# Optimization experiments

Measured on AMD Instinct MI355X. Metric: run time of the kernel, lower is better.

Reference implementation:

```python
import jax, jax.numpy as jnp
import numpy as np


def setup_inputs() -> dict:
    key = jax.random.key(0)
    k1, k2, k3, k4 = jax.random.split(key, 4)
    B, T, E, D = 4, 4096, 2048, 128
    x = jax.random.normal(k1, (B, T, E), dtype=jnp.float32)
    # nn.Linear(E, D, bias=False): y = x @ W where W is [E, D]
    scale = 1.0 / np.sqrt(E)
    Wq = jax.random.normal(k2, (E, D), dtype=jnp.float32) * scale
    Wk = jax.random.normal(k3, (E, D), dtype=jnp.float32) * scale
    Wv = jax.random.normal(k4, (E, D), dtype=jnp.float32) * scale
    return {"x": x, "Wq": Wq, "Wk": Wk, "Wv": Wv}


def reference(x, Wq, Wk, Wv):
    # Single attention head, prefill path (kv_cache=None, T_q == T_k).
    D = Wq.shape[1]
    Q = jnp.einsum('bte,ed->btd', x, Wq)
    K = jnp.einsum('bte,ed->btd', x, Wk)
    V = jnp.einsum('bte,ed->btd', x, Wv)
    scores = jnp.einsum('bqd,bkd->bqk', Q, K) / jnp.sqrt(jnp.float32(D))
    T = x.shape[1]
    causal = jnp.tril(jnp.ones((T, T), dtype=bool))  # [T_q, T_k]
    scores = jnp.where(causal[None, :, :], scores, -jnp.inf)
    attn = jax.nn.softmax(scores, axis=-1)
    out = jnp.einsum('bqk,bkd->bqd', attn, V)
    return out
```

## Files before the change

### kernel.cpp

```cpp
#include <hip/hip_runtime.h>
#include <hip/hip_bf16.h>

typedef short bf16x8 __attribute__((ext_vector_type(8)));
typedef float f32x4  __attribute__((ext_vector_type(4)));

#define T_SEQ 4096
#define NB    4
#define E_DIM 2048
#define D_DIM 128
#define M_TOT (NB * T_SEQ)
#define NCHUNK 4
#define CHUNK_KT 16
#define SM_SHIFT 12.0f

__device__ __forceinline__ ushort f2bf(float f) {
  union { float f; unsigned u; } c; c.f = f;
  unsigned u = c.u;
  unsigned r = (u + 0x7FFFu + ((u >> 16) & 1u)) >> 16;
  return (ushort)r;
}
__device__ __forceinline__ float bf2f(ushort u) {
  union { unsigned u; float f; } c; c.u = ((unsigned)u) << 16;
  return c.f;
}
__device__ __forceinline__ bf16x8 cvt8(const float4& lo, const float4& hi) {
  union { __hip_bfloat162 h; ushort u[2]; } t;
  union { ushort u[8]; bf16x8 v; } r;
  t.h = __float22bfloat162_rn(make_float2(lo.x, lo.y)); r.u[0] = t.u[0]; r.u[1] = t.u[1];
  t.h = __float22bfloat162_rn(make_float2(lo.z, lo.w)); r.u[2] = t.u[0]; r.u[3] = t.u[1];
  t.h = __float22bfloat162_rn(make_float2(hi.x, hi.y)); r.u[4] = t.u[0]; r.u[5] = t.u[1];
  t.h = __float22bfloat162_rn(make_float2(hi.z, hi.w)); r.u[6] = t.u[0]; r.u[7] = t.u[1];
  return r.v;
}

__device__ __forceinline__ void gl2lds16(const void* g, void* l) {
  __builtin_amdgcn_global_load_lds(
      (const __attribute__((address_space(1))) unsigned int*)g,
      (__attribute__((address_space(3))) unsigned int*)l, 16, 0, 0);
}

__global__ __launch_bounds__(256) void build_wt(const float* __restrict__ Wq,
                                                const float* __restrict__ Wk,
                                                const float* __restrict__ Wv,
                                                ushort* __restrict__ Wt) {
  __shared__ ushort tile[64][72];
  const int tid = threadIdx.x;
  const int k0 = blockIdx.x * 64, n0 = blockIdx.y * 64, o = blockIdx.z;
  const float* W = (o == 0) ? Wq : ((o == 1) ? Wk : Wv);
  for (int i = 0; i < 4; i++) {
    int c = tid + i * 256;
    int r = c >> 4, c4 = (c & 15) * 4;
    float4 v = *(const float4*)(W + (size_t)(k0 + r) * D_DIM + n0 + c4);
    ushort4 b4;
    b4.x = f2bf(v.x); b4.y = f2bf(v.y); b4.z = f2bf(v.z); b4.w = f2bf(v.w);
    *(ushort4*)(&tile[r][c4]) = b4;
  }
  __syncthreads();
  for (int i = 0; i < 2; i++) {
    int c = tid + i * 256;
    int nn = c >> 3, k8 = (c & 7) * 8;
    ushort tmp[8];
    for (int j = 0; j < 8; j++) tmp[j] = tile[k8 + j][nn];
    *(uint4*)(Wt + (size_t)((o << 7) + n0 + nn) * E_DIM + k0 + k8) = *(const uint4*)tmp;
  }
}

__global__ __launch_bounds__(256) void qkv_gemm(const float* __restrict__ x,
                                                const ushort* __restrict__ Wt,
                                                ushort* __restrict__ Q,
                                                ushort* __restrict__ K,
                                                ushort* __restrict__ V) {
  __shared__ ushort Bs[2][192 * 64];

  const int tid  = threadIdx.x;
  const int wave = tid >> 6, lane = tid & 63;
  const int quad = lane >> 4, l16 = lane & 15;
  const int wm = wave >> 1, wn = wave & 1;
  const int m0 = blockIdx.x * 64;
  const int n0 = blockIdx.y * 192;

  f32x4 acc[2][6] = {};

  const int s_   = wave * 64 + lane;
  const int n_   = s_ >> 3, p_ = s_ & 7;

#define DMA_B(k0_, buf_)                                                        \
  for (int i_ = 0; i_ < 6; i_++) {                                              \
    int slotbase = i_ * 256 + wave * 64;                                        \
    int n = (i_ * 256 >> 3) + n_;       \
    int cg = p_ ^ (n & 7);                                                      \
    gl2lds16(Wt + (size_t)(n0 + n) * E_DIM + (k0_) + cg * 8,                    \
             (char*)(buf_) + (size_t)slotbase * 16);                            \
  }

  DMA_B(0, Bs[0]);
  __syncthreads();

  const float* xbase = x + (size_t)(m0 + wm * 32 + l16) * E_DIM + quad * 8;

  for (int it = 0; it < 32; it++) {
    const int k0 = it * 64;
    if (it < 31) { DMA_B(k0 + 64, Bs[(it + 1) & 1]); }
    const ushort* bs = Bs[it & 1];

    float4 a4[2][2][2];
    for (int mi = 0; mi < 2; mi++)
      for (int kk = 0; kk < 2; kk++) {
        const float* ap = xbase + (size_t)mi * 16 * E_DIM + k0 + kk * 32;
        a4[mi][kk][0] = *(const float4*)ap;
        a4[mi][kk][1] = *(const float4*)(ap + 4);
      }

    for (int kk = 0; kk < 2; kk++) {
      bf16x8 af[2];
      af[0] = cvt8(a4[0][kk][0], a4[0][kk][1]);
      af[1] = cvt8(a4[1][kk][0], a4[1][kk][1]);
      const int sw = ((kk * 4 + quad) ^ (l16 & 7)) * 8;
      for (int ni = 0; ni < 6; ni++) {
        int n = wn * 96 + ni * 16 + l16;
        bf16x8 bf = *(const bf16x8*)(bs + n * 64 + sw);
        acc[0][ni] = __builtin_amdgcn_mfma_f32_16x16x32_bf16(af[0], bf, acc[0][ni], 0, 0, 0);
        acc[1][ni] = __builtin_amdgcn_mfma_f32_16x16x32_bf16(af[1], bf, acc[1][ni], 0, 0, 0);
      }
    }
    __syncthreads();
  }

  for (int mi = 0; mi < 2; mi++)
    for (int ni = 0; ni < 6; ni++) {
      int colall = n0 + wn * 96 + ni * 16 + l16;
      int o = colall >> 7, d = colall & 127;
      ushort* dst = (o == 0) ? Q : ((o == 1) ? K : V);
      for (int r = 0; r < 4; r++) {
        int row = m0 + wm * 32 + mi * 16 + quad * 4 + r;
        dst[(size_t)row * D_DIM + d] = f2bf(acc[mi][ni][r]);
      }
    }
#undef DMA_B
}

__global__ __launch_bounds__(256) void v_transpose(const ushort* __restrict__ V,
                                                   ushort* __restrict__ Vt) {
  __shared__ ushort tile[64][72];
  const int tid = threadIdx.x;
  const int t0 = blockIdx.x * 64, d0 = blockIdx.y * 64, b = blockIdx.z;
  for (int i = 0; i < 2; i++) {
    int c = tid + i * 256;
    int r = c >> 3, cc = (c & 7) * 8;
    *(uint4*)(&tile[r][cc]) = *(const uint4*)(V + (size_t)(b * T_SEQ + t0 + r) * D_DIM + d0 + cc);
  }
  __syncthreads();
  for (int i = 0; i < 2; i++) {
    int c = tid + i * 256;
    int dr = c >> 3, tc = (c & 7) * 8;
    ushort tmp[8];
    for (int j = 0; j < 8; j++) tmp[j] = tile[tc + j][dr];
    *(uint4*)(Vt + (size_t)(b * D_DIM + d0 + dr) * T_SEQ + t0 + tc) = *(const uint4*)tmp;
  }
}

__global__ __launch_bounds__(256) void attn_partial(const ushort* __restrict__ Q,
                                                    const ushort* __restrict__ K,
                                                    const ushort* __restrict__ Vt,
                                                    ushort* __restrict__ Po,
                                                    float* __restrict__ Ll) {
  const int qt = blockIdx.x, cq = blockIdx.y, b = blockIdx.z;
  const int kt0 = cq * CHUNK_KT;
  if (kt0 > qt) return;

  __shared__ ushort Kt[64][136];
  __shared__ ushort Vts[128][72];
  __shared__ ushort Pls[4][16][72];

  const int tid = threadIdx.x;
  const int wave = tid >> 6, lane = tid & 63;
  const int quad = lane >> 4, l16 = lane & 15;

  const int qrow = qt * 64 + wave * 16 + l16;
  bf16x8 qf[4];
  for (int kk = 0; kk < 4; kk++)
    qf[kk] = *(const bf16x8*)(Q + (size_t)(b * T_SEQ + qrow) * D_DIM + kk * 32 + quad * 8);

  bf16x8 ones;
  for (int j = 0; j < 8; j++) ones[j] = (short)0x3F80;

  f32x4 o_acc[8] = {};
  f32x4 lacc = {};
  const float scale2 = 0.08838834764831845f * 1.4426950408889634f;

  const int kt1 = min(qt, kt0 + CHUNK_KT - 1);

  for (int kt = kt0; kt <= kt1; kt++) {
    __syncthreads();
    for (int i = 0; i < 4; i++) {
      int c = tid + i * 256;
      int r = c >> 4, col = (c & 15) * 8;
      *(uint4*)(&Kt[r][col]) = *(const uint4*)(K + (size_t)(b * T_SEQ + kt * 64 + r) * D_DIM + col);
    }
    for (int i = 0; i < 4; i++) {
      int c = tid + i * 256;
      int dr = c >> 3, col = (c & 7) * 8;
      *(uint4*)(&Vts[dr][col]) = *(const uint4*)(Vt + (size_t)(b * D_DIM + dr) * T_SEQ + kt * 64 + col);
    }
    __syncthreads();

    f32x4 s[4] = {};
    for (int kk = 0; kk < 4; kk++) {
      const int kc = kk * 32 + quad * 8;
      for (int ni = 0; ni < 4; ni++) {
        bf16x8 bf = *(const bf16x8*)(&Kt[ni * 16 + l16][kc]);
        s[ni] = __builtin_amdgcn_mfma_f32_16x16x32_bf16(qf[kk], bf, s[ni], 0, 0, 0);
      }
    }
    if (kt == qt) {
      for (int ni = 0; ni < 4; ni++) {
        int kidx = kt * 64 + ni * 16 + l16;
        for (int r = 0; r < 4; r++) {
          int qidx = qt * 64 + wave * 16 + quad * 4 + r;
          float v = (kidx > qidx) ? -1e30f : (s[ni][r] * scale2 - SM_SHIFT);
          s[ni][r] = exp2f(v);
        }
      }
    } else {
      for (int ni = 0; ni < 4; ni++)
        for (int r = 0; r < 4; r++)
          s[ni][r] = exp2f(s[ni][r] * scale2 - SM_SHIFT);
    }
    for (int ni = 0; ni < 4; ni++)
      for (int r = 0; r < 4; r++)
        Pls[wave][quad * 4 + r][ni * 16 + l16] = f2bf(s[ni][r]);
    for (int kk2 = 0; kk2 < 2; kk2++) {
      const int kc = kk2 * 32 + quad * 8;
      bf16x8 pf = *(const bf16x8*)(&Pls[wave][l16][kc]);
      for (int ni = 0; ni < 8; ni++) {
        bf16x8 vf = *(const bf16x8*)(&Vts[ni * 16 + l16][kc]);
        o_acc[ni] = __builtin_amdgcn_mfma_f32_16x16x32_bf16(pf, vf, o_acc[ni], 0, 0, 0);
      }
      lacc = __builtin_amdgcn_mfma_f32_16x16x32_bf16(pf, ones, lacc, 0, 0, 0);
    }
  }

  const int slot = (b * 64 + qt) * NCHUNK + cq;
  for (int ni = 0; ni < 8; ni++)
    for (int r = 0; r < 4; r++) {
      int ql = wave * 16 + quad * 4 + r;
      Po[(size_t)slot * 8192 + ql * D_DIM + ni * 16 + l16] = f2bf(o_acc[ni][r]);
    }
  if (l16 == 0) {
    for (int r = 0; r < 4; r++) {
      int ql = wave * 16 + quad * 4 + r;
      Ll[slot * 64 + ql] = lacc[r];
    }
  }
}

__global__ __launch_bounds__(256) void attn_reduce(const ushort* __restrict__ Po,
                                                   const float* __restrict__ Ll,
                                                   float* __restrict__ out) {
  const int qt = blockIdx.x, b = blockIdx.y;
  const int nc = qt / CHUNK_KT + 1;
  const int tid = threadIdx.x;
  const int row = tid >> 2;
  const int c0  = (tid & 3) * 32;
  const int base_slot = (b * 64 + qt) * NCHUNK;

  float L = 0.f;
  for (int c = 0; c < nc; c++) L += Ll[(base_slot + c) * 64 + row];
  const float inv = 1.0f / L;

  const size_t orow = (size_t)(b * T_SEQ + qt * 64 + row) * D_DIM;
  for (int cc = 0; cc < 32; cc += 8) {
    float a[8] = {0,0,0,0,0,0,0,0};
    for (int c = 0; c < nc; c++) {
      const ushort* p = Po + (size_t)(base_slot + c) * 8192 + row * D_DIM + c0 + cc;
      ushort u[8];
      *(uint4*)u = *(const uint4*)p;
      for (int j = 0; j < 8; j++) a[j] += bf2f(u[j]);
    }
    float4 o0, o1;
    o0.x = a[0] * inv; o0.y = a[1] * inv; o0.z = a[2] * inv; o0.w = a[3] * inv;
    o1.x = a[4] * inv; o1.y = a[5] * inv; o1.z = a[6] * inv; o1.w = a[7] * inv;
    *(float4*)(out + orow + c0 + cc)     = o0;
    *(float4*)(out + orow + c0 + cc + 4) = o1;
  }
}

extern "C" void kernel_launch(void* const* d_in, const int* in_sizes, int n_in,
                              void* d_out, int out_size, void* d_ws, size_t ws_size,
                              hipStream_t stream) {
  const float* x  = (const float*)d_in[0];
  const float* Wq = (const float*)d_in[1];
  const float* Wk = (const float*)d_in[2];
  const float* Wv = (const float*)d_in[3];
  float* out = (float*)d_out;

  ushort* Q  = (ushort*)d_ws;
  ushort* Kb = Q  + (size_t)M_TOT * D_DIM;
  ushort* Vb = Kb + (size_t)M_TOT * D_DIM;
  ushort* Vt = Vb + (size_t)M_TOT * D_DIM;
  ushort* Wt = Vt + (size_t)M_TOT * D_DIM;
  ushort* Po = Wt + (size_t)384 * E_DIM;
  float*  Ll = (float*)(Po + (size_t)NB * 64 * NCHUNK * 8192);

  hipLaunchKernelGGL(build_wt,     dim3(32, 2, 3),       dim3(256), 0, stream, Wq, Wk, Wv, Wt);
  hipLaunchKernelGGL(qkv_gemm,     dim3(256, 2),         dim3(256), 0, stream, x, Wt, Q, Kb, Vb);
  hipLaunchKernelGGL(v_transpose,  dim3(64, 2, 4),       dim3(256), 0, stream, Vb, Vt);
  hipLaunchKernelGGL(attn_partial, dim3(64, NCHUNK, 4),  dim3(256), 0, stream, Q, Kb, Vt, Po, Ll);
  hipLaunchKernelGGL(attn_reduce,  dim3(64, 4),          dim3(256), 0, stream, Po, Ll, out);
}
```

Measured before the change: 299.5 us.

## Pre-pack weights, K and V into MFMA fragment layout and drop LDS staging

```diff
diff --git a/kernel.cpp b/kernel.cpp
--- a/kernel.cpp
+++ b/kernel.cpp
@@ -9,8 +9,6 @@
 #define E_DIM 2048
 #define D_DIM 128
 #define M_TOT (NB * T_SEQ)
-#define NCHUNK 4
-#define CHUNK_KT 16
 #define SM_SHIFT 12.0f
 
 __device__ __forceinline__ ushort f2bf(float f) {
@@ -32,46 +30,47 @@
   t.h = __float22bfloat162_rn(make_float2(hi.z, hi.w)); r.u[6] = t.u[0]; r.u[7] = t.u[1];
   return r.v;
 }
-
-__device__ __forceinline__ void gl2lds16(const void* g, void* l) {
-  __builtin_amdgcn_global_load_lds(
-      (const __attribute__((address_space(1))) unsigned int*)g,
-      (__attribute__((address_space(3))) unsigned int*)l, 16, 0, 0);
-}
-
-__global__ __launch_bounds__(256) void build_wt(const float* __restrict__ Wq,
-                                                const float* __restrict__ Wk,
-                                                const float* __restrict__ Wv,
-                                                ushort* __restrict__ Wt) {
+__device__ __forceinline__ bf16x8 ld_frag(const ushort* p) {
+  union { uint4 q; bf16x8 v; } u;
+  u.q = *(const uint4*)p;
+  return u.v;
+}
+
+__global__ __launch_bounds__(256) void build_wtp(const float* __restrict__ Wq,
+                                                 const float* __restrict__ Wk,
+                                                 const float* __restrict__ Wv,
+                                                 ushort* __restrict__ Wtp) {
   __shared__ ushort tile[64][72];
   const int tid = threadIdx.x;
-  const int k0 = blockIdx.x * 64, n0 = blockIdx.y * 64, o = blockIdx.z;
+  const int wave = tid >> 6, lane = tid & 63;
+  const int quad = lane >> 4, l16 = lane & 15;
+  const int k0 = blockIdx.x * 64, nl0 = blockIdx.y * 64, o = blockIdx.z;
   const float* W = (o == 0) ? Wq : ((o == 1) ? Wk : Wv);
   for (int i = 0; i < 4; i++) {
     int c = tid + i * 256;
     int r = c >> 4, c4 = (c & 15) * 4;
-    float4 v = *(const float4*)(W + (size_t)(k0 + r) * D_DIM + n0 + c4);
+    float4 v = *(const float4*)(W + (size_t)(k0 + r) * D_DIM + nl0 + c4);
     ushort4 b4;
     b4.x = f2bf(v.x); b4.y = f2bf(v.y); b4.z = f2bf(v.z); b4.w = f2bf(v.w);
     *(ushort4*)(&tile[r][c4]) = b4;
   }
   __syncthreads();
-  for (int i = 0; i < 2; i++) {
-    int c = tid + i * 256;
-    int nn = c >> 3, k8 = (c & 7) * 8;
+  for (int j = 0; j < 2; j++) {
+    int f = wave * 2 + j;
+    int ntl = f >> 1, ktl = f & 1;
     ushort tmp[8];
-    for (int j = 0; j < 8; j++) tmp[j] = tile[k8 + j][nn];
-    *(uint4*)(Wt + (size_t)((o << 7) + n0 + nn) * E_DIM + k0 + k8) = *(const uint4*)tmp;
+    for (int jj = 0; jj < 8; jj++) tmp[jj] = tile[ktl * 32 + quad * 8 + jj][ntl * 16 + l16];
+    int ntg = o * 8 + (nl0 >> 4) + ntl;
+    int ktg = (k0 >> 5) + ktl;
+    *(uint4*)(Wtp + (size_t)(ntg * 64 + ktg) * 512 + lane * 8) = *(const uint4*)tmp;
   }
 }
 
 __global__ __launch_bounds__(256) void qkv_gemm(const float* __restrict__ x,
-                                                const ushort* __restrict__ Wt,
+                                                const ushort* __restrict__ Wtp,
                                                 ushort* __restrict__ Q,
                                                 ushort* __restrict__ K,
                                                 ushort* __restrict__ V) {
-  __shared__ ushort Bs[2][192 * 64];
-
   const int tid  = threadIdx.x;
   const int wave = tid >> 6, lane = tid & 63;
   const int quad = lane >> 4, l16 = lane & 15;
@@ -81,49 +80,26 @@
 
   f32x4 acc[2][6] = {};
 
-  const int s_   = wave * 64 + lane;
-  const int n_   = s_ >> 3, p_ = s_ & 7;
-
-#define DMA_B(k0_, buf_)                                                        \
-  for (int i_ = 0; i_ < 6; i_++) {                                              \
-    int slotbase = i_ * 256 + wave * 64;                                        \
-    int n = (i_ * 256 >> 3) + n_;       \
-    int cg = p_ ^ (n & 7);                                                      \
-    gl2lds16(Wt + (size_t)(n0 + n) * E_DIM + (k0_) + cg * 8,                    \
-             (char*)(buf_) + (size_t)slotbase * 16);                            \
-  }
-
-  DMA_B(0, Bs[0]);
-  __syncthreads();
-
-  const float* xbase = x + (size_t)(m0 + wm * 32 + l16) * E_DIM + quad * 8;
-
-  for (int it = 0; it < 32; it++) {
-    const int k0 = it * 64;
-    if (it < 31) { DMA_B(k0 + 64, Bs[(it + 1) & 1]); }
-    const ushort* bs = Bs[it & 1];
-
-    float4 a4[2][2][2];
-    for (int mi = 0; mi < 2; mi++)
-      for (int kk = 0; kk < 2; kk++) {
-        const float* ap = xbase + (size_t)mi * 16 * E_DIM + k0 + kk * 32;
-        a4[mi][kk][0] = *(const float4*)ap;
-        a4[mi][kk][1] = *(const float4*)(ap + 4);
-      }
-
-    for (int kk = 0; kk < 2; kk++) {
-      bf16x8 af[2];
-      af[0] = cvt8(a4[0][kk][0], a4[0][kk][1]);
-      af[1] = cvt8(a4[1][kk][0], a4[1][kk][1]);
-      const int sw = ((kk * 4 + quad) ^ (l16 & 7)) * 8;
-      for (int ni = 0; ni < 6; ni++) {
-        int n = wn * 96 + ni * 16 + l16;
-        bf16x8 bf = *(const bf16x8*)(bs + n * 64 + sw);
-        acc[0][ni] = __builtin_amdgcn_mfma_f32_16x16x32_bf16(af[0], bf, acc[0][ni], 0, 0, 0);
-        acc[1][ni] = __builtin_amdgcn_mfma_f32_16x16x32_bf16(af[1], bf, acc[1][ni], 0, 0, 0);
-      }
-    }
-    __syncthreads();
+  const float* xb0 = x + (size_t)(m0 + wm * 32 + l16) * E_DIM + quad * 8;
+  const float* xb1 = xb0 + (size_t)16 * E_DIM;
+  const int ntbase = (n0 >> 4) + wn * 6;
+
+  for (int kt = 0; kt < 64; kt++) {
+    float4 a0l = *(const float4*)(xb0 + kt * 32);
+    float4 a0h = *(const float4*)(xb0 + kt * 32 + 4);
+    float4 a1l = *(const float4*)(xb1 + kt * 32);
+    float4 a1h = *(const float4*)(xb1 + kt * 32 + 4);
+    bf16x8 bf[6];
+#pragma unroll
+    for (int ni = 0; ni < 6; ni++)
+      bf[ni] = ld_frag(Wtp + (size_t)((ntbase + ni) * 64 + kt) * 512 + lane * 8);
+    bf16x8 af0 = cvt8(a0l, a0h);
+    bf16x8 af1 = cvt8(a1l, a1h);
+#pragma unroll
+    for (int ni = 0; ni < 6; ni++) {
+      acc[0][ni] = __builtin_amdgcn_mfma_f32_16x16x32_bf16(af0, bf[ni], acc[0][ni], 0, 0, 0);
+      acc[1][ni] = __builtin_amdgcn_mfma_f32_16x16x32_bf16(af1, bf[ni], acc[1][ni], 0, 0, 0);
+    }
   }
 
   for (int mi = 0; mi < 2; mi++)
@@ -136,143 +112,178 @@
         dst[(size_t)row * D_DIM + d] = f2bf(acc[mi][ni][r]);
       }
     }
-#undef DMA_B
-}
-
-__global__ __launch_bounds__(256) void v_transpose(const ushort* __restrict__ V,
-                                                   ushort* __restrict__ Vt) {
-  __shared__ ushort tile[64][72];
-  const int tid = threadIdx.x;
-  const int t0 = blockIdx.x * 64, d0 = blockIdx.y * 64, b = blockIdx.z;
-  for (int i = 0; i < 2; i++) {
+}
+
+__global__ __launch_bounds__(256) void k_pack(const ushort* __restrict__ K,
+                                              ushort* __restrict__ Kp) {
+  const int tid = threadIdx.x;
+  const int wave = tid >> 6, lane = tid & 63;
+  const int quad = lane >> 4, l16 = lane & 15;
+  const int t0 = blockIdx.x * 64, b = blockIdx.y;
+  for (int j = 0; j < 4; j++) {
+    int f = wave * 4 + j;
+    int ntl = f >> 2, ktd = f & 3;
+    uint4 v = *(const uint4*)(K + (size_t)(b * T_SEQ + t0 + ntl * 16 + l16) * D_DIM + ktd * 32 + quad * 8);
+    *(uint4*)(Kp + (size_t)(((b * 256 + (t0 >> 4) + ntl) * 4) + ktd) * 512 + lane * 8) = v;
+  }
+}
+
+__global__ __launch_bounds__(256) void v_pack(const ushort* __restrict__ V,
+                                              ushort* __restrict__ Vp) {
+  __shared__ ushort tile[64][136];
+  const int tid = threadIdx.x;
+  const int wave = tid >> 6, lane = tid & 63;
+  const int quad = lane >> 4, l16 = lane & 15;
+  const int t0 = blockIdx.x * 64, b = blockIdx.y;
+  for (int i = 0; i < 4; i++) {
     int c = tid + i * 256;
-    int r = c >> 3, cc = (c & 7) * 8;
-    *(uint4*)(&tile[r][cc]) = *(const uint4*)(V + (size_t)(b * T_SEQ + t0 + r) * D_DIM + d0 + cc);
+    int r = c >> 4, cc = (c & 15) * 8;
+    *(uint4*)(&tile[r][cc]) = *(const uint4*)(V + (size_t)(b * T_SEQ + t0 + r) * D_DIM + cc);
   }
   __syncthreads();
-  for (int i = 0; i < 2; i++) {
-    int c = tid + i * 256;
-    int dr = c >> 3, tc = (c & 7) * 8;
+  for (int j = 0; j < 4; j++) {
+    int f = wave * 4 + j;
+    int ntd = f >> 1, ktt = f & 1;
     ushort tmp[8];
-    for (int j = 0; j < 8; j++) tmp[j] = tile[tc + j][dr];
-    *(uint4*)(Vt + (size_t)(b * D_DIM + d0 + dr) * T_SEQ + t0 + tc) = *(const uint4*)tmp;
-  }
-}
-
-__global__ __launch_bounds__(256) void attn_partial(const ushort* __restrict__ Q,
-                                                    const ushort* __restrict__ K,
-                                                    const ushort* __restrict__ Vt,
-                                                    ushort* __restrict__ Po,
-                                                    float* __restrict__ Ll) {
+    for (int jj = 0; jj < 8; jj++) tmp[jj] = tile[ktt * 32 + quad * 8 + jj][ntd * 16 + l16];
+    *(uint4*)(Vp + (size_t)((b * 8 + ntd) * 128 + (t0 >> 5) + ktt) * 512 + lane * 8) = *(const uint4*)tmp;
+  }
+}
+
+__global__ void attn_partial(const ushort* __restrict__ Q,
+                             const ushort* __restrict__ Kp,
+                             const ushort* __restrict__ Vp,
+                             ushort* __restrict__ Po,
+                             float* __restrict__ Ll,
+                             int chunkKT, int nchunk) {
   const int qt = blockIdx.x, cq = blockIdx.y, b = blockIdx.z;
-  const int kt0 = cq * CHUNK_KT;
-  if (kt0 > qt) return;
-
-  __shared__ ushort Kt[64][136];
-  __shared__ ushort Vts[128][72];
-  __shared__ ushort Pls[4][16][72];
-
-  const int tid = threadIdx.x;
-  const int wave = tid >> 6, lane = tid & 63;
-  const int quad = lane >> 4, l16 = lane & 15;
-
-  const int qrow = qt * 64 + wave * 16 + l16;
-  bf16x8 qf[4];
-  for (int kk = 0; kk < 4; kk++)
-    qf[kk] = *(const bf16x8*)(Q + (size_t)(b * T_SEQ + qrow) * D_DIM + kk * 32 + quad * 8);
+  const int ktmax = qt * 2 + 1;
+  const int kt0 = cq * chunkKT;
+  if (kt0 > ktmax) return;
+  const int kt1 = min(ktmax, kt0 + chunkKT - 1);
+
+  __shared__ ushort Pls[4][32][72];
+
+  const int tid = threadIdx.x;
+  const int wave = tid >> 6, lane = tid & 63;
+  const int quad = lane >> 4, l16 = lane & 15;
+
+  bf16x8 qf[2][4];
+  for (int mi = 0; mi < 2; mi++) {
+    const ushort* qp = Q + (size_t)(b * T_SEQ + qt * 128 + wave * 32 + mi * 16 + l16) * D_DIM + quad * 8;
+    for (int kk = 0; kk < 4; kk++) qf[mi][kk] = ld_frag(qp + kk * 32);
+  }
 
   bf16x8 ones;
   for (int j = 0; j < 8; j++) ones[j] = (short)0x3F80;
 
-  f32x4 o_acc[8] = {};
-  f32x4 lacc = {};
+  f32x4 o_acc[2][8] = {};
+  f32x4 lacc[2] = {};
   const float scale2 = 0.08838834764831845f * 1.4426950408889634f;
 
-  const int kt1 = min(qt, kt0 + CHUNK_KT - 1);
+  const ushort* Kpb = Kp + (size_t)b * 256 * 4 * 512;
+  const ushort* Vpb = Vp + (size_t)b * 8 * 128 * 512;
 
   for (int kt = kt0; kt <= kt1; kt++) {
-    __syncthreads();
-    for (int i = 0; i < 4; i++) {
-      int c = tid + i * 256;
-      int r = c >> 4, col = (c & 15) * 8;
-      *(uint4*)(&Kt[r][col]) = *(const uint4*)(K + (size_t)(b * T_SEQ + kt * 64 + r) * D_DIM + col);
-    }
-    for (int i = 0; i < 4; i++) {
-      int c = tid + i * 256;
-      int dr = c >> 3, col = (c & 7) * 8;
-      *(uint4*)(&Vts[dr][col]) = *(const uint4*)(Vt + (size_t)(b * D_DIM + dr) * T_SEQ + kt * 64 + col);
-    }
-    __syncthreads();
-
-    f32x4 s[4] = {};
-    for (int kk = 0; kk < 4; kk++) {
-      const int kc = kk * 32 + quad * 8;
+    bf16x8 kf[16];
+#pragma unroll
+    for (int kk = 0; kk < 4; kk++)
+#pragma unroll
+      for (int ni = 0; ni < 4; ni++)
+        kf[kk * 4 + ni] = ld_frag(Kpb + (size_t)((kt * 4 + ni) * 4 + kk) * 512 + lane * 8);
+    f32x4 s[2][4] = {};
+#pragma unroll
+    for (int kk = 0; kk < 4; kk++)
+#pragma unroll
       for (int ni = 0; ni < 4; ni++) {
-        bf16x8 bf = *(const bf16x8*)(&Kt[ni * 16 + l16][kc]);
-        s[ni] = __builtin_amdgcn_mfma_f32_16x16x32_bf16(qf[kk], bf, s[ni], 0, 0, 0);
-      }
-    }
-    if (kt == qt) {
-      for (int ni = 0; ni < 4; ni++) {
-        int kidx = kt * 64 + ni * 16 + l16;
-        for (int r = 0; r < 4; r++) {
-          int qidx = qt * 64 + wave * 16 + quad * 4 + r;
-          float v = (kidx > qidx) ? -1e30f : (s[ni][r] * scale2 - SM_SHIFT);
-          s[ni][r] = exp2f(v);
+        s[0][ni] = __builtin_amdgcn_mfma_f32_16x16x32_bf16(qf[0][kk], kf[kk * 4 + ni], s[0][ni], 0, 0, 0);
+        s[1][ni] = __builtin_amdgcn_mfma_f32_16x16x32_bf16(qf[1][kk], kf[kk * 4 + ni], s[1][ni], 0, 0, 0);
+      }
+    if (kt >= qt * 2) {
+#pragma unroll
+      for (int mi = 0; mi < 2; mi++)
+#pragma unroll
+        for (int ni = 0; ni < 4; ni++) {
+          int kidx = kt * 64 + ni * 16 + l16;
+#pragma unroll
+          for (int r = 0; r < 4; r++) {
+            int qidx = qt * 128 + wave * 32 + mi * 16 + quad * 4 + r;
+            float v = (kidx > qidx) ? -1e30f : (s[mi][ni][r] * scale2 - SM_SHIFT);
+            s[mi][ni][r] = exp2f(v);
+          }
         }
-      }
     } else {
+#pragma unroll
+      for (int mi = 0; mi < 2; mi++)
+#pragma unroll
+        for (int ni = 0; ni < 4; ni++)
+#pragma unroll
+          for (int r = 0; r < 4; r++)
+            s[mi][ni][r] = exp2f(s[mi][ni][r] * scale2 - SM_SHIFT);
+    }
+#pragma unroll
+    for (int mi = 0; mi < 2; mi++)
+#pragma unroll
       for (int ni = 0; ni < 4; ni++)
+#pragma unroll
         for (int r = 0; r < 4; r++)
-          s[ni][r] = exp2f(s[ni][r] * scale2 - SM_SHIFT);
-    }
-    for (int ni = 0; ni < 4; ni++)
-      for (int r = 0; r < 4; r++)
-        Pls[wave][quad * 4 + r][ni * 16 + l16] = f2bf(s[ni][r]);
+          Pls[wave][mi * 16 + quad * 4 + r][ni * 16 + l16] = f2bf(s[mi][ni][r]);
+    bf16x8 vf[16];
+#pragma unroll
+    for (int kk2 = 0; kk2 < 2; kk2++)
+#pragma unroll
+      for (int ni = 0; ni < 8; ni++)
+        vf[kk2 * 8 + ni] = ld_frag(Vpb + (size_t)(ni * 128 + kt * 2 + kk2) * 512 + lane * 8);
+#pragma unroll
     for (int kk2 = 0; kk2 < 2; kk2++) {
-      const int kc = kk2 * 32 + quad * 8;
-      bf16x8 pf = *(const bf16x8*)(&Pls[wave][l16][kc]);
+      bf16x8 pf[2];
+      pf[0] = *(const bf16x8*)(&Pls[wave][l16][kk2 * 32 + quad * 8]);
+      pf[1] = *(const bf16x8*)(&Pls[wave][16 + l16][kk2 * 32 + quad * 8]);
+#pragma unroll
       for (int ni = 0; ni < 8; ni++) {
-        bf16x8 vf = *(const bf16x8*)(&Vts[ni * 16 + l16][kc]);
-        o_acc[ni] = __builtin_amdgcn_mfma_f32_16x16x32_bf16(pf, vf, o_acc[ni], 0, 0, 0);
-      }
-      lacc = __builtin_amdgcn_mfma_f32_16x16x32_bf16(pf, ones, lacc, 0, 0, 0);
-    }
-  }
-
-  const int slot = (b * 64 + qt) * NCHUNK + cq;
-  for (int ni = 0; ni < 8; ni++)
-    for (int r = 0; r < 4; r++) {
-      int ql = wave * 16 + quad * 4 + r;
-      Po[(size_t)slot * 8192 + ql * D_DIM + ni * 16 + l16] = f2bf(o_acc[ni][r]);
-    }
-  if (l16 == 0) {
-    for (int r = 0; r < 4; r++) {
-      int ql = wave * 16 + quad * 4 + r;
-      Ll[slot * 64 + ql] = lacc[r];
-    }
-  }
+        o_acc[0][ni] = __builtin_amdgcn_mfma_f32_16x16x32_bf16(pf[0], vf[kk2 * 8 + ni], o_acc[0][ni], 0, 0, 0);
+        o_acc[1][ni] = __builtin_amdgcn_mfma_f32_16x16x32_bf16(pf[1], vf[kk2 * 8 + ni], o_acc[1][ni], 0, 0, 0);
+      }
+      lacc[0] = __builtin_amdgcn_mfma_f32_16x16x32_bf16(pf[0], ones, lacc[0], 0, 0, 0);
+      lacc[1] = __builtin_amdgcn_mfma_f32_16x16x32_bf16(pf[1], ones, lacc[1], 0, 0, 0);
+    }
+  }
+
+  const int slot = (b * 32 + qt) * nchunk + cq;
+  for (int mi = 0; mi < 2; mi++)
+    for (int ni = 0; ni < 8; ni++)
+      for (int r = 0; r < 4; r++) {
+        int row = wave * 32 + mi * 16 + quad * 4 + r;
+        Po[(size_t)slot * 16384 + row * D_DIM + ni * 16 + l16] = f2bf(o_acc[mi][ni][r]);
+      }
+  if (l16 == 0)
+    for (int mi = 0; mi < 2; mi++)
+      for (int r = 0; r < 4; r++) {
+        int row = wave * 32 + mi * 16 + quad * 4 + r;
+        Ll[slot * 128 + row] = lacc[mi][r];
+      }
 }
 
 __global__ __launch_bounds__(256) void attn_reduce(const ushort* __restrict__ Po,
                                                    const float* __restrict__ Ll,
-                                                   float* __restrict__ out) {
+                                                   float* __restrict__ out,
+                                                   int chunkKT, int nchunk) {
   const int qt = blockIdx.x, b = blockIdx.y;
-  const int nc = qt / CHUNK_KT + 1;
-  const int tid = threadIdx.x;
-  const int row = tid >> 2;
-  const int c0  = (tid & 3) * 32;
-  const int base_slot = (b * 64 + qt) * NCHUNK;
+  const int nc = (qt * 2 + 1) / chunkKT + 1;
+  const int tid = threadIdx.x;
+  const int row = tid >> 1;
+  const int c0  = (tid & 1) * 64;
+  const int base_slot = (b * 32 + qt) * nchunk;
 
   float L = 0.f;
-  for (int c = 0; c < nc; c++) L += Ll[(base_slot + c) * 64 + row];
+  for (int c = 0; c < nc; c++) L += Ll[(base_slot + c) * 128 + row];
   const float inv = 1.0f / L;
 
-  const size_t orow = (size_t)(b * T_SEQ + qt * 64 + row) * D_DIM;
-  for (int cc = 0; cc < 32; cc += 8) {
+  const size_t orow = (size_t)(b * T_SEQ + qt * 128 + row) * D_DIM;
+  for (int cc = 0; cc < 64; cc += 8) {
     float a[8] = {0,0,0,0,0,0,0,0};
     for (int c = 0; c < nc; c++) {
-      const ushort* p = Po + (size_t)(base_slot + c) * 8192 + row * D_DIM + c0 + cc;
+      const ushort* p = Po + (size_t)(base_slot + c) * 16384 + row * D_DIM + c0 + cc;
       ushort u[8];
       *(uint4*)u = *(const uint4*)p;
       for (int j = 0; j < 8; j++) a[j] += bf2f(u[j]);
@@ -294,17 +305,26 @@
   const float* Wv = (const float*)d_in[3];
   float* out = (float*)d_out;
 
-  ushort* Q  = (ushort*)d_ws;
-  ushort* Kb = Q  + (size_t)M_TOT * D_DIM;
-  ushort* Vb = Kb + (size_t)M_TOT * D_DIM;
-  ushort* Vt = Vb + (size_t)M_TOT * D_DIM;
-  ushort* Wt = Vt + (size_t)M_TOT * D_DIM;
-  ushort* Po = Wt + (size_t)384 * E_DIM;
-  float*  Ll = (float*)(Po + (size_t)NB * 64 * NCHUNK * 8192);
-
-  hipLaunchKernelGGL(build_wt,     dim3(32, 2, 3),       dim3(256), 0, stream, Wq, Wk, Wv, Wt);
-  hipLaunchKernelGGL(qkv_gemm,     dim3(256, 2),         dim3(256), 0, stream, x, Wt, Q, Kb, Vb);
-  hipLaunchKernelGGL(v_transpose,  dim3(64, 2, 4),       dim3(256), 0, stream, Vb, Vt);
-  hipLaunchKernelGGL(attn_partial, dim3(64, NCHUNK, 4),  dim3(256), 0, stream, Q, Kb, Vt, Po, Ll);
-  hipLaunchKernelGGL(attn_reduce,  dim3(64, 4),          dim3(256), 0, stream, Po, Ll, out);
-}
+  const size_t nQKV = (size_t)M_TOT * D_DIM;
+  ushort* Q   = (ushort*)d_ws;
+  ushort* Kb  = Q   + nQKV;
+  ushort* Vb  = Kb  + nQKV;
+  ushort* Wtp = Vb  + nQKV;
+  ushort* Kp  = Wtp + (size_t)384 * E_DIM;
+  ushort* Vp  = Kp  + nQKV;
+  ushort* Po  = Vp  + nQKV;
+
+  size_t fixed_bytes = ((size_t)5 * nQKV + (size_t)384 * E_DIM) * 2;
+  size_t per_chunk   = (size_t)NB * 32 * (16384 * 2 + 128 * 4);
+  int nchunk = 8;
+  while (nchunk > 2 && fixed_bytes + (size_t)nchunk * per_chunk > ws_size) nchunk >>= 1;
+  const int chunkKT = 64 / nchunk;
+  float* Ll = (float*)(Po + (size_t)NB * 32 * nchunk * 16384);
+
+  hipLaunchKernelGGL(build_wtp,    dim3(32, 2, 3),        dim3(256), 0, stream, Wq, Wk, Wv, Wtp);
+  hipLaunchKernelGGL(qkv_gemm,     dim3(256, 2),          dim3(256), 0, stream, x, Wtp, Q, Kb, Vb);
+  hipLaunchKernelGGL(k_pack,       dim3(64, NB),          dim3(256), 0, stream, Kb, Kp);
+  hipLaunchKernelGGL(v_pack,       dim3(64, NB),          dim3(256), 0, stream, Vb, Vp);
+  hipLaunchKernelGGL(attn_partial, dim3(32, nchunk, NB),  dim3(256), 0, stream, Q, Kp, Vp, Po, Ll, chunkKT, nchunk);
+  hipLaunchKernelGGL(attn_reduce,  dim3(32, NB),          dim3(256), 0, stream, Po, Ll, out, chunkKT, nchunk);
+}
```

Result: slower. 419.5 us (+40.1%).
